# Optimization experiments

Measured on AMD Instinct MI355X. Metric: run time of the kernel, lower is better.

Reference implementation:

```python
import jax, jax.numpy as jnp
import numpy as np

DIM = 512
NH, NKV, HD = 8, 4, DIM // 8
KVD = NKV * HD
EPS = 1.1920928955078125e-07  # torch.finfo(float32).eps (F.rms_norm default)
ROPE_BASE = 10000.0


def _rms_norm(x):
    # F.rms_norm over last dim, no learned weight
    ms = jnp.mean(jnp.square(x), axis=-1, keepdims=True)
    return x * jax.lax.rsqrt(ms + EPS)


def _rope_tables(T, dtype):
    inv_freq = 1.0 / (ROPE_BASE ** (jnp.arange(0, HD, 2, dtype=jnp.float32) / HD))
    t = jnp.arange(T, dtype=jnp.float32)
    f = jnp.outer(t, inv_freq)  # [T, HD//2]
    return jnp.cos(f).astype(dtype)[None, None], jnp.sin(f).astype(dtype)[None, None]


def _apply_rot(x, c, s):
    h = x.shape[-1] // 2
    x1, x2 = x[..., :h], x[..., h:]
    return jnp.concatenate((x1 * c + x2 * s, -x1 * s + x2 * c), axis=-1)


def setup_inputs() -> dict:
    key = jax.random.key(0)
    ks = jax.random.split(key, 5)
    B, T = 8, 2048
    x = jax.random.normal(ks[0], (B, T, DIM), dtype=jnp.float32)
    # torch Linear weights: [out_features, in_features]
    Wq = jax.random.normal(ks[1], (DIM, DIM), dtype=jnp.float32) * (DIM ** -0.5)
    Wk = jax.random.normal(ks[2], (KVD, DIM), dtype=jnp.float32) * (DIM ** -0.5)
    Wv = jax.random.normal(ks[3], (KVD, DIM), dtype=jnp.float32) * (DIM ** -0.5)
    Wp = jax.random.normal(ks[4], (DIM, DIM), dtype=jnp.float32) * (DIM ** -0.5)
    return {"x": x, "Wq": Wq, "Wk": Wk, "Wv": Wv, "Wp": Wp}


def reference(x, Wq, Wk, Wv, Wp):
    B, T, C = x.shape
    q = (x @ Wq.T).reshape(B, T, NH, HD).transpose(0, 2, 1, 3)    # [B,NH,T,HD]
    k = (x @ Wk.T).reshape(B, T, NKV, HD).transpose(0, 2, 1, 3)   # [B,NKV,T,HD]
    v = (x @ Wv.T).reshape(B, T, NKV, HD).transpose(0, 2, 1, 3)
    q, k = _rms_norm(q), _rms_norm(k)
    c, s = _rope_tables(T, q.dtype)
    q, k = _apply_rot(q, c, s), _apply_rot(k, c, s)
    rep = NH // NKV
    k = jnp.repeat(k, rep, axis=1)  # GQA expand -> [B,NH,T,HD]
    v = jnp.repeat(v, rep, axis=1)
    scale = 1.0 / jnp.sqrt(jnp.asarray(HD, dtype=q.dtype))
    scores = jnp.einsum('bhqd,bhkd->bhqk', q, k) * scale
    causal = jnp.tril(jnp.ones((T, T), dtype=bool))
    scores = jnp.where(causal[None, None], scores, jnp.finfo(scores.dtype).min)
    attn = jax.nn.softmax(scores, axis=-1)
    y = jnp.einsum('bhqk,bhkd->bhqd', attn, v)
    y = y.transpose(0, 2, 1, 3).reshape(B, T, C)
    return y @ Wp.T
```

## Files before the change

kernel.cpp:

```cpp
#include <hip/hip_runtime.h>
#include <hip/hip_bf16.h>
#include <stdint.h>

typedef __bf16 bf16;
typedef __bf16 bf16x8 __attribute__((ext_vector_type(8)));
typedef __bf16 bf16x4 __attribute__((ext_vector_type(4)));
typedef float f32x4 __attribute__((ext_vector_type(4)));

#define T_SEQ 2048
#define DIM_ 512
#define NH_ 8
#define NKV_ 4
#define HD_ 64
#define BT_ (8 * T_SEQ)
#define NEG_INF (-1e30f)
#define EPS_ 1.1920928955078125e-07f
#define QSCALE 0.18033688011112042f
#define SMAX 12.0f

#define OFF_XB   (size_t)(0)
#define OFF_WQKV (size_t)(16777216)
#define OFF_WP   (size_t)(17825792)
#define OFF_COS  (size_t)(18350080)
#define OFF_SIN  (size_t)(18612224)
#define OFF_QT   (size_t)(18874368)
#define OFF_KT   (size_t)(35651584)
#define OFF_VT   (size_t)(44040192)
#define OFF_Y    (size_t)(52428800)
#define WS_NEEDED (size_t)(69206016)

__device__ inline void mfma16(f32x4& acc, bf16x8 a, bf16x8 b) {
    acc = __builtin_amdgcn_mfma_f32_16x16x32_bf16(a, b, acc, 0, 0, 0);
}

typedef const __attribute__((address_space(1))) uint8_t* gas_ptr;
typedef __attribute__((address_space(3))) uint8_t* las_ptr;
__device__ inline void gload16(const bf16* g, bf16* l) {
    __builtin_amdgcn_global_load_lds((gas_ptr)(const void*)g, (las_ptr)(void*)l, 16, 0, 0);
}

__device__ inline bf16x4 cvt4(const float4& a) {
    bf16x4 v;
    v[0] = (bf16)a.x; v[1] = (bf16)a.y; v[2] = (bf16)a.z; v[3] = (bf16)a.w;
    return v;
}

__global__ void prep_kernel(const float* __restrict__ x, const float* __restrict__ wq,
                            const float* __restrict__ wk, const float* __restrict__ wv,
                            const float* __restrict__ wp,
                            bf16* __restrict__ xb, bf16* __restrict__ wqkv,
                            bf16* __restrict__ wpb, float* __restrict__ cosT,
                            float* __restrict__ sinT) {
    int tid = blockIdx.x * blockDim.x + threadIdx.x;
    int stride = gridDim.x * blockDim.x;
    for (int i = tid; i < BT_ * DIM_ / 4; i += stride)
        *(bf16x4*)(xb + (size_t)i * 4) = cvt4(((const float4*)x)[i]);
    for (int i = tid; i < 1024 * 512 / 4; i += stride) {
        int e = i * 4;
        int j = e >> 9, k = e & 511;
        const float* src;
        if (j < 512) src = wq + (size_t)j * 512 + k;
        else if (j < 768) src = wk + (size_t)(j - 512) * 512 + k;
        else src = wv + (size_t)(j - 768) * 512 + k;
        *(bf16x4*)(wqkv + (size_t)e) = cvt4(*(const float4*)src);
    }
    for (int i = tid; i < 512 * 512 / 4; i += stride)
        *(bf16x4*)(wpb + (size_t)i * 4) = cvt4(((const float4*)wp)[i]);
    for (int i = tid; i < T_SEQ * 32; i += stride) {
        int t = i >> 5, d = i & 31;
        float inv = powf(10000.0f, -(float)d * (1.0f / 32.0f));
        float f = (float)t * inv;
        cosT[i] = cosf(f);
        sinT[i] = sinf(f);
    }
}

__global__ __launch_bounds__(512, 4) void qkv_gemm(const bf16* __restrict__ A,
                                                   const bf16* __restrict__ B,
                                                   bf16* __restrict__ qt,
                                                   bf16* __restrict__ kt,
                                                   bf16* __restrict__ vt,
                                                   const float* __restrict__ cosT,
                                                   const float* __restrict__ sinT) {
    __shared__ __align__(16) char smem[49152];
    bf16* As = (bf16*)smem;
    bf16* Bs = (bf16*)(smem + 32768);
    const int tid = threadIdx.x, lane = tid & 63, wid = tid >> 6;
    const int wr = wid >> 1, wc = wid & 1;
    const int lm = lane & 15, hi = lane >> 4;
    const int bid = blockIdx.x;
    const int swz = (bid & 7) * 64 + (bid >> 3);
    const int brow = (swz & 63) * 256;
    const int bcol = (swz >> 6) * 128;

    f32x4 acc[4][4] = {};
    for (int k0 = 0; k0 < 512; k0 += 64) {
        __syncthreads();
#pragma unroll
        for (int i = 0; i < 4; ++i) {
            int c = i * 512 + tid;
            int f = c >> 6, l = c & 63;
            int row = (f >> 1) * 16 + (l & 15);
            int kc = (f & 1) * 32 + (l >> 4) * 8;
            gload16(A + (size_t)(brow + row) * 512 + k0 + kc, As + c * 8);
        }
#pragma unroll
        for (int i = 0; i < 2; ++i) {
            int c = i * 512 + tid;
            int f = c >> 6, l = c & 63;
            int row = (f >> 1) * 16 + (l & 15);
            int kc = (f & 1) * 32 + (l >> 4) * 8;
            gload16(B + (size_t)(bcol + row) * 512 + k0 + kc, Bs + c * 8);
        }
        asm volatile("s_waitcnt vmcnt(0)" ::: "memory");
        __syncthreads();
#pragma unroll
        for (int kk = 0; kk < 2; ++kk) {
            bf16x8 af[4], bfr[4];
#pragma unroll
            for (int m = 0; m < 4; ++m)
                af[m] = *(const bf16x8*)(As + (((wr * 4 + m) * 2 + kk) * 64 + lane) * 8);
#pragma unroll
            for (int n = 0; n < 4; ++n)
                bfr[n] = *(const bf16x8*)(Bs + (((wc * 4 + n) * 2 + kk) * 64 + lane) * 8);
            __builtin_amdgcn_s_setprio(1);
#pragma unroll
            for (int m = 0; m < 4; ++m)
#pragma unroll
                for (int n = 0; n < 4; ++n) mfma16(acc[m][n], af[m], bfr[n]);
            __builtin_amdgcn_s_setprio(0);
        }
    }
    __syncthreads();

    bf16* Tb = (bf16*)smem + wid * 2112;
    const int wcol = bcol + wc * 64;
    const int ctype = (wcol < 512) ? 0 : (wcol < 768 ? 1 : 2);
    const int i0 = brow + wr * 64;
    const int b = i0 >> 11, tt = i0 & (T_SEQ - 1);

#pragma unroll
    for (int h2 = 0; h2 < 2; ++h2) {
        if (ctype < 2) {
#pragma unroll
            for (int mm = 0; mm < 2; ++mm) {
                const int m = h2 * 2 + mm;
#pragma unroll
                for (int r = 0; r < 4; ++r) {
                    float v0 = acc[m][0][r], v1 = acc[m][1][r];
                    float v2 = acc[m][2][r], v3 = acc[m][3][r];
                    float ss = v0 * v0 + v1 * v1 + v2 * v2 + v3 * v3;
                    ss += __shfl_xor(ss, 1);
                    ss += __shfl_xor(ss, 2);
                    ss += __shfl_xor(ss, 4);
                    ss += __shfl_xor(ss, 8);
                    float rinv = rsqrtf(ss * (1.0f / 64.0f) + EPS_);
                    v0 *= rinv; v1 *= rinv; v2 *= rinv; v3 *= rinv;
                    int rl = m * 16 + hi * 4 + r;
                    int t = (i0 + rl) & (T_SEQ - 1);
                    float c0 = cosT[t * 32 + lm], s0 = sinT[t * 32 + lm];
                    float c1 = cosT[t * 32 + 16 + lm], s1 = sinT[t * 32 + 16 + lm];
                    float o0 = v0 * c0 + v2 * s0;
                    float o2 = v2 * c0 - v0 * s0;
                    float o1 = v1 * c1 + v3 * s1;
                    float o3 = v3 * c1 - v1 * s1;
                    if (ctype == 0) { o0 *= QSCALE; o1 *= QSCALE; o2 *= QSCALE; o3 *= QSCALE; }
                    int rloc = mm * 16 + hi * 4 + r;
                    Tb[rloc * 66 + lm]      = (bf16)o0;
                    Tb[rloc * 66 + 16 + lm] = (bf16)o1;
                    Tb[rloc * 66 + 32 + lm] = (bf16)o2;
                    Tb[rloc * 66 + 48 + lm] = (bf16)o3;
                }
            }
        } else {
#pragma unroll
            for (int m = 0; m < 4; ++m)
#pragma unroll
                for (int nn = 0; nn < 2; ++nn) {
                    const int n = h2 * 2 + nn;
#pragma unroll
                    for (int r = 0; r < 4; ++r)
                        Tb[(nn * 16 + lm) * 66 + m * 16 + hi * 4 + r] = (bf16)acc[m][n][r];
                }
        }
#pragma unroll
        for (int pp = 0; pp < 4; ++pp) {
            int row = pp * 8 + (lane >> 3);
            int ch = lane & 7;
            bf16x8 val = *(const bf16x8*)(Tb + row * 66 + ch * 8);
            if (ctype == 0) {
                int head = wcol >> 6;
                *(bf16x8*)(qt + ((size_t)((b << 3) + head) * T_SEQ + tt + h2 * 32 + row) * 64 + ch * 8) = val;
            } else if (ctype == 1) {
                int head = (wcol - 512) >> 6;
                *(bf16x8*)(kt + ((size_t)((b << 2) + head) * T_SEQ + tt + h2 * 32 + row) * 64 + ch * 8) = val;
            } else {
                int head = (wcol - 768) >> 6;
                *(bf16x8*)(vt + ((size_t)((b << 2) + head) * 64 + h2 * 32 + row) * T_SEQ + tt + ch * 8) = val;
            }
        }
    }
}

__global__ __launch_bounds__(512, 4) void attn_kernel(const bf16* __restrict__ qt,
                                                      const bf16* __restrict__ kt,
                                                      const bf16* __restrict__ vt,
                                                      bf16* __restrict__ y) {
    __shared__ bf16 Klds[4096];
    __shared__ bf16 Vlds[4096];
    __shared__ bf16 Plds[8][1152];
    const int tid = threadIdx.x;
    const int lane = tid & 63, wid = tid >> 6;
    const int lm = lane & 15, hi = lane >> 4;
    const int bid = blockIdx.x;
    const int s4 = bid >> 8;
    const int g4 = (bid >> 6) & 3;
    const int bh = bid & 63;
    const int p = 4 * (3 - s4) + ((g4 + s4) & 3);
    const int b = bh >> 3, h = bh & 7, hv = h >> 1;
    const bf16* Q = qt + (size_t)bh * T_SEQ * HD_;
    const bf16* K = kt + (size_t)(b * NKV_ + hv) * T_SEQ * HD_;
    const bf16* V = vt + (size_t)(b * NKV_ + hv) * HD_ * T_SEQ;
    const int qB = p * 128;
    const int qw = qB + wid * 16;
    bf16* Pl = &Plds[wid][0];

    const int sl0 = tid >> 6, l0 = tid & 63;
    const int gr0 = (sl0 >> 1) * 16 + (l0 & 15);
    const int gc0 = (sl0 & 1) * 32 + (l0 >> 4) * 8;
    const bf16* kg0 = K + (size_t)gr0 * HD_ + gc0;
    const bf16* vg0 = V + (size_t)gr0 * T_SEQ + gc0;
    bf16* kd0 = Klds + (size_t)tid * 8;
    bf16* vd0 = Vlds + (size_t)tid * 8;

    bf16x8 qf[2];
#pragma unroll
    for (int kk = 0; kk < 2; ++kk)
        qf[kk] = *(const bf16x8*)(Q + (size_t)(qw + lm) * HD_ + 32 * kk + 8 * hi);

    bf16x8 vones;
#pragma unroll
    for (int j = 0; j < 8; ++j) vones[j] = (bf16)1.0f;

    f32x4 o[4] = {};
    f32x4 lacc = {};

    const int nt = (qB >> 6) + 2;
    for (int t = 0; t < nt; ++t) {
        const int kv0 = t << 6;
        __syncthreads();
        {
            size_t ko = (size_t)kv0 * HD_, vo = (size_t)kv0;
            gload16(kg0 + ko, kd0);
            gload16(vg0 + vo, vd0);
        }
        asm volatile("s_waitcnt vmcnt(0)" ::: "memory");
        __syncthreads();

        if (kv0 <= qw + 15) {
            f32x4 s[4] = {};
#pragma unroll
            for (int kk = 0; kk < 2; ++kk) {
                bf16x8 kf[4];
#pragma unroll
                for (int n = 0; n < 4; ++n)
                    kf[n] = *(const bf16x8*)(Klds + ((n * 2 + kk) * 64 + lane) * 8);
                __builtin_amdgcn_s_setprio(1);
#pragma unroll
                for (int n = 0; n < 4; ++n) mfma16(s[n], kf[n], qf[kk]);
                __builtin_amdgcn_s_setprio(0);
            }
            const bool partial = (kv0 + 63 > qw);
            const int qg = qw + lm;
            bf16x4 pw[4];
#pragma unroll
            for (int n = 0; n < 4; ++n)
#pragma unroll
                for (int r = 0; r < 4; ++r) {
                    float xv = s[n][r];
                    if (partial)
                        xv = ((kv0 + 16 * n + 4 * hi + r) <= qg) ? xv : NEG_INF;
                    pw[n][r] = (bf16)__builtin_amdgcn_exp2f(xv - SMAX);
                }
#pragma unroll
            for (int kk = 0; kk < 2; ++kk) {
                *(bf16x4*)(Pl + lm * 40 + 4 * hi)      = pw[2 * kk];
                *(bf16x4*)(Pl + lm * 40 + 16 + 4 * hi) = pw[2 * kk + 1];
                bf16x8 vf[4], pf;
                pf = *(const bf16x8*)(Pl + lm * 40 + 8 * hi);
#pragma unroll
                for (int nd = 0; nd < 4; ++nd)
                    vf[nd] = *(const bf16x8*)(Vlds + ((nd * 2 + kk) * 64 + lane) * 8);
                __builtin_amdgcn_s_setprio(1);
#pragma unroll
                for (int nd = 0; nd < 4; ++nd) mfma16(o[nd], vf[nd], pf);
                mfma16(lacc, vones, pf);
                __builtin_amdgcn_s_setprio(0);
            }
        }
    }

    float rcl = 1.0f / lacc[0];
#pragma unroll
    for (int nd = 0; nd < 4; ++nd) {
        bf16x4 ov;
#pragma unroll
        for (int r = 0; r < 4; ++r) ov[r] = (bf16)(o[nd][r] * rcl);
        *(bf16x4*)(Pl + lm * 72 + nd * 16 + 4 * hi) = ov;
    }
#pragma unroll
    for (int it = 0; it < 2; ++it) {
        int chunk = it * 64 + lane;
        int row = chunk >> 3, dc = (chunk & 7) * 8;
        bf16x8 val = *(const bf16x8*)(Pl + row * 72 + dc);
        *(bf16x8*)(y + (size_t)(b * T_SEQ + qw + row) * DIM_ + h * HD_ + dc) = val;
    }
}

__global__ __launch_bounds__(256) void proj_gemm(const bf16* __restrict__ A,
                                                 const bf16* __restrict__ B,
                                                 float* __restrict__ out) {
    __shared__ __align__(16) char smem[32768];
    bf16* As = (bf16*)smem;
    bf16* Bs = (bf16*)(smem + 16384);
    const int tid = threadIdx.x, lane = tid & 63, wid = tid >> 6;
    const int wr = wid >> 1, wc = wid & 1;
    const int lm = lane & 15, hi = lane >> 4;
    const int bid = blockIdx.x;
    const int swz = (bid & 7) * 64 + (bid >> 3);
    const int brow = (swz & 127) * 128;
    const int bcol = (swz >> 7) * 128;

    f32x4 acc[4][4] = {};
    for (int k0 = 0; k0 < 512; k0 += 64) {
        __syncthreads();
#pragma unroll
        for (int i = 0; i < 4; ++i) {
            int c = i * 256 + tid;
            int slot = c >> 6, l = c & 63;
            int row = (slot >> 1) * 16 + (l & 15);
            int kc = (slot & 1) * 32 + (l >> 4) * 8;
            gload16(A + (size_t)(brow + row) * 512 + k0 + kc, As + c * 8);
            gload16(B + (size_t)(bcol + row) * 512 + k0 + kc, Bs + c * 8);
        }
        asm volatile("s_waitcnt vmcnt(0)" ::: "memory");
        __syncthreads();
#pragma unroll
        for (int kk = 0; kk < 2; ++kk) {
            bf16x8 af[4], bfr[4];
#pragma unroll
            for (int m = 0; m < 4; ++m)
                af[m] = *(const bf16x8*)(As + (((wr * 4 + m) * 2 + kk) * 64 + lane) * 8);
#pragma unroll
            for (int n = 0; n < 4; ++n)
                bfr[n] = *(const bf16x8*)(Bs + (((wc * 4 + n) * 2 + kk) * 64 + lane) * 8);
            __builtin_amdgcn_s_setprio(1);
#pragma unroll
            for (int m = 0; m < 4; ++m)
#pragma unroll
                for (int n = 0; n < 4; ++n) mfma16(acc[m][n], af[m], bfr[n]);
            __builtin_amdgcn_s_setprio(0);
        }
    }
#pragma unroll
    for (int m = 0; m < 4; ++m)
#pragma unroll
        for (int n = 0; n < 4; ++n)
#pragma unroll
            for (int r = 0; r < 4; ++r) {
                int i = brow + wr * 64 + m * 16 + hi * 4 + r;
                int j = bcol + wc * 64 + n * 16 + lm;
                out[(size_t)i * DIM_ + j] = acc[m][n][r];
            }
}

extern "C" void kernel_launch(void* const* d_in, const int* in_sizes, int n_in,
                              void* d_out, int out_size, void* d_ws, size_t ws_size,
                              hipStream_t stream) {
    const float* x  = (const float*)d_in[0];
    const float* wq = (const float*)d_in[1];
    const float* wk = (const float*)d_in[2];
    const float* wv = (const float*)d_in[3];
    const float* wp = (const float*)d_in[4];
    if (ws_size < WS_NEEDED) return;

    char* ws = (char*)d_ws;
    bf16* xb    = (bf16*)(ws + OFF_XB);
    bf16* wqkv  = (bf16*)(ws + OFF_WQKV);
    bf16* wpb   = (bf16*)(ws + OFF_WP);
    float* cosT = (float*)(ws + OFF_COS);
    float* sinT = (float*)(ws + OFF_SIN);
    bf16* qt    = (bf16*)(ws + OFF_QT);
    bf16* kt    = (bf16*)(ws + OFF_KT);
    bf16* vt    = (bf16*)(ws + OFF_VT);
    bf16* y     = (bf16*)(ws + OFF_Y);

    prep_kernel<<<2048, 256, 0, stream>>>(x, wq, wk, wv, wp, xb, wqkv, wpb, cosT, sinT);

    qkv_gemm<<<512, 512, 0, stream>>>(xb, wqkv, qt, kt, vt, cosT, sinT);

    attn_kernel<<<1024, 512, 0, stream>>>(qt, kt, vt, y);

    proj_gemm<<<512, 256, 0, stream>>>(y, wpb, (float*)d_out);
}
```

Measured before the change: 127.2 us.

## Process two 16-row query tiles per wave in attention to reuse K/V fragments

Each wave in the attention kernel now handles 32 query rows instead of 16, so a block covers 256 queries and the grid drops from 1024 to 512 blocks. K and V fragments loaded from LDS are shared across two query sub-tiles, doubling MFMA work per LDS read and per global K/V tile load. The block-to-query-tile mapping is changed to pair heavy and light causal tiles. This raises register pressure, halves the number of blocks available for occupancy, and widens the causal imbalance within each block.

```diff
diff --git a/kernel.cpp b/kernel.cpp
--- a/kernel.cpp
+++ b/kernel.cpp
@@ -208,21 +208,21 @@
                                                       bf16* __restrict__ y) {
     __shared__ bf16 Klds[4096];
     __shared__ bf16 Vlds[4096];
-    __shared__ bf16 Plds[8][1152];
+    __shared__ bf16 Plds[8][1280];
     const int tid = threadIdx.x;
     const int lane = tid & 63, wid = tid >> 6;
     const int lm = lane & 15, hi = lane >> 4;
     const int bid = blockIdx.x;
-    const int s4 = bid >> 8;
+    const int s2 = bid >> 8;
     const int g4 = (bid >> 6) & 3;
     const int bh = bid & 63;
-    const int p = 4 * (3 - s4) + ((g4 + s4) & 3);
+    const int p = (s2 == 0) ? (7 - g4) : g4;
     const int b = bh >> 3, h = bh & 7, hv = h >> 1;
     const bf16* Q = qt + (size_t)bh * T_SEQ * HD_;
     const bf16* K = kt + (size_t)(b * NKV_ + hv) * T_SEQ * HD_;
     const bf16* V = vt + (size_t)(b * NKV_ + hv) * HD_ * T_SEQ;
-    const int qB = p * 128;
-    const int qw = qB + wid * 16;
+    const int qB = p * 256;
+    const int qw = qB + wid * 32;
     bf16* Pl = &Plds[wid][0];
 
     const int sl0 = tid >> 6, l0 = tid & 63;
@@ -233,19 +233,21 @@
     bf16* kd0 = Klds + (size_t)tid * 8;
     bf16* vd0 = Vlds + (size_t)tid * 8;
 
-    bf16x8 qf[2];
-#pragma unroll
-    for (int kk = 0; kk < 2; ++kk)
-        qf[kk] = *(const bf16x8*)(Q + (size_t)(qw + lm) * HD_ + 32 * kk + 8 * hi);
+    bf16x8 qf[2][2];
+#pragma unroll
+    for (int qm = 0; qm < 2; ++qm)
+#pragma unroll
+        for (int kk = 0; kk < 2; ++kk)
+            qf[qm][kk] = *(const bf16x8*)(Q + (size_t)(qw + 16 * qm + lm) * HD_ + 32 * kk + 8 * hi);
 
     bf16x8 vones;
 #pragma unroll
     for (int j = 0; j < 8; ++j) vones[j] = (bf16)1.0f;
 
-    f32x4 o[4] = {};
-    f32x4 lacc = {};
-
-    const int nt = (qB >> 6) + 2;
+    f32x4 o[2][4] = {};
+    f32x4 lacc[2] = {};
+
+    const int nt = (qB >> 6) + 4;
     for (int t = 0; t < nt; ++t) {
         const int kv0 = t << 6;
         __syncthreads();
@@ -257,8 +259,8 @@
         asm volatile("s_waitcnt vmcnt(0)" ::: "memory");
         __syncthreads();
 
-        if (kv0 <= qw + 15) {
-            f32x4 s[4] = {};
+        if (kv0 <= qw + 31) {
+            f32x4 s[2][4] = {};
 #pragma unroll
             for (int kk = 0; kk < 2; ++kk) {
                 bf16x8 kf[4];
@@ -267,53 +269,70 @@
                     kf[n] = *(const bf16x8*)(Klds + ((n * 2 + kk) * 64 + lane) * 8);
                 __builtin_amdgcn_s_setprio(1);
 #pragma unroll
-                for (int n = 0; n < 4; ++n) mfma16(s[n], kf[n], qf[kk]);
+                for (int qm = 0; qm < 2; ++qm)
+#pragma unroll
+                    for (int n = 0; n < 4; ++n) mfma16(s[qm][n], kf[n], qf[qm][kk]);
                 __builtin_amdgcn_s_setprio(0);
             }
             const bool partial = (kv0 + 63 > qw);
-            const int qg = qw + lm;
-            bf16x4 pw[4];
-#pragma unroll
-            for (int n = 0; n < 4; ++n)
-#pragma unroll
-                for (int r = 0; r < 4; ++r) {
-                    float xv = s[n][r];
-                    if (partial)
-                        xv = ((kv0 + 16 * n + 4 * hi + r) <= qg) ? xv : NEG_INF;
-                    pw[n][r] = (bf16)__builtin_amdgcn_exp2f(xv - SMAX);
+            bf16x4 pw[2][4];
+#pragma unroll
+            for (int qm = 0; qm < 2; ++qm) {
+                const int qg = qw + 16 * qm + lm;
+#pragma unroll
+                for (int n = 0; n < 4; ++n)
+#pragma unroll
+                    for (int r = 0; r < 4; ++r) {
+                        float xv = s[qm][n][r];
+                        if (partial)
+                            xv = ((kv0 + 16 * n + 4 * hi + r) <= qg) ? xv : NEG_INF;
+                        pw[qm][n][r] = (bf16)__builtin_amdgcn_exp2f(xv - SMAX);
+                    }
+            }
+#pragma unroll
+            for (int kk = 0; kk < 2; ++kk) {
+#pragma unroll
+                for (int qm = 0; qm < 2; ++qm) {
+                    *(bf16x4*)(Pl + (16 * qm + lm) * 40 + 4 * hi)      = pw[qm][2 * kk];
+                    *(bf16x4*)(Pl + (16 * qm + lm) * 40 + 16 + 4 * hi) = pw[qm][2 * kk + 1];
                 }
-#pragma unroll
-            for (int kk = 0; kk < 2; ++kk) {
-                *(bf16x4*)(Pl + lm * 40 + 4 * hi)      = pw[2 * kk];
-                *(bf16x4*)(Pl + lm * 40 + 16 + 4 * hi) = pw[2 * kk + 1];
-                bf16x8 vf[4], pf;
-                pf = *(const bf16x8*)(Pl + lm * 40 + 8 * hi);
+                bf16x8 vf[4], pf[2];
+#pragma unroll
+                for (int qm = 0; qm < 2; ++qm)
+                    pf[qm] = *(const bf16x8*)(Pl + (16 * qm + lm) * 40 + 8 * hi);
 #pragma unroll
                 for (int nd = 0; nd < 4; ++nd)
                     vf[nd] = *(const bf16x8*)(Vlds + ((nd * 2 + kk) * 64 + lane) * 8);
                 __builtin_amdgcn_s_setprio(1);
 #pragma unroll
-                for (int nd = 0; nd < 4; ++nd) mfma16(o[nd], vf[nd], pf);
-                mfma16(lacc, vones, pf);
+                for (int qm = 0; qm < 2; ++qm)
+#pragma unroll
+                    for (int nd = 0; nd < 4; ++nd) mfma16(o[qm][nd], vf[nd], pf[qm]);
+#pragma unroll
+                for (int qm = 0; qm < 2; ++qm)
+                    mfma16(lacc[qm], vones, pf[qm]);
                 __builtin_amdgcn_s_setprio(0);
             }
         }
     }
 
-    float rcl = 1.0f / lacc[0];
-#pragma unroll
-    for (int nd = 0; nd < 4; ++nd) {
-        bf16x4 ov;
-#pragma unroll
-        for (int r = 0; r < 4; ++r) ov[r] = (bf16)(o[nd][r] * rcl);
-        *(bf16x4*)(Pl + lm * 72 + nd * 16 + 4 * hi) = ov;
-    }
-#pragma unroll
-    for (int it = 0; it < 2; ++it) {
-        int chunk = it * 64 + lane;
-        int row = chunk >> 3, dc = (chunk & 7) * 8;
-        bf16x8 val = *(const bf16x8*)(Pl + row * 72 + dc);
-        *(bf16x8*)(y + (size_t)(b * T_SEQ + qw + row) * DIM_ + h * HD_ + dc) = val;
+#pragma unroll
+    for (int qm = 0; qm < 2; ++qm) {
+        float rcl = 1.0f / lacc[qm][0];
+#pragma unroll
+        for (int nd = 0; nd < 4; ++nd) {
+            bf16x4 ov;
+#pragma unroll
+            for (int r = 0; r < 4; ++r) ov[r] = (bf16)(o[qm][nd][r] * rcl);
+            *(bf16x4*)(Pl + lm * 72 + nd * 16 + 4 * hi) = ov;
+        }
+#pragma unroll
+        for (int it = 0; it < 2; ++it) {
+            int chunk = it * 64 + lane;
+            int row = chunk >> 3, dc = (chunk & 7) * 8;
+            bf16x8 val = *(const bf16x8*)(Pl + row * 72 + dc);
+            *(bf16x8*)(y + (size_t)(b * T_SEQ + qw + 16 * qm + row) * DIM_ + h * HD_ + dc) = val;
+        }
     }
 }
 
@@ -399,7 +418,7 @@
 
     qkv_gemm<<<512, 512, 0, stream>>>(xb, wqkv, qt, kt, vt, cosT, sinT);
 
-    attn_kernel<<<1024, 512, 0, stream>>>(qt, kt, vt, y);
+    attn_kernel<<<512, 512, 0, stream>>>(qt, kt, vt, y);
 
     proj_gemm<<<512, 256, 0, stream>>>(y, wpb, (float*)d_out);
 }
```

Measured after the change: 140.3 us. +10.3%, slower.
